# Kernel optimization log

Measured on AMD Instinct MI355X. Metric: run time of the kernel, lower is better.

## Reference

```python
import jax, jax.numpy as jnp
import numpy as np

D_IN = 4096
NUM_HEADS = 32
HEAD_DIM = 128
NUM_KV = 8
GROUP = NUM_HEADS // NUM_KV
EPS = 1e-6
ROPE_BASE = 10000.0


def rms_norm(x, scale):
    # norm over last dim (head_dim), computed in fp32 as in torch ref
    var = jnp.mean(x * x, axis=-1, keepdims=True)
    return x * jax.lax.rsqrt(var + EPS) * scale


def rope_cos_sin(positions, dim):
    inv_freq = 1.0 / (ROPE_BASE ** (jnp.arange(0, dim, 2, dtype=jnp.float32) / dim))
    angles = positions.astype(jnp.float32)[:, None] * inv_freq[None, :]  # (N, dim/2)
    angles = jnp.concatenate([angles, angles], axis=-1)  # (N, dim)
    return jnp.cos(angles), jnp.sin(angles)


def apply_rope(t, cos, sin):
    # t: (N, heads, D); cos/sin: (N, D)
    half = t.shape[-1] // 2
    rot = jnp.concatenate([-t[..., half:], t[..., :half]], axis=-1)
    return t * cos[:, None, :] + rot * sin[:, None, :]


def setup_inputs() -> dict:
    key = jax.random.key(0)
    ks = jax.random.split(key, 6)
    B, S = 1, 2048
    x = jax.random.normal(ks[0], (B, S, D_IN), dtype=jnp.float32)
    positions = jnp.arange(B * S, dtype=jnp.int32)
    sc = 0.02
    Wq = jax.random.normal(ks[1], (D_IN, NUM_HEADS * HEAD_DIM), dtype=jnp.float32) * sc
    Wk = jax.random.normal(ks[2], (D_IN, NUM_KV * HEAD_DIM), dtype=jnp.float32) * sc
    Wv = jax.random.normal(ks[3], (D_IN, NUM_KV * HEAD_DIM), dtype=jnp.float32) * sc
    Wo = jax.random.normal(ks[4], (NUM_HEADS * HEAD_DIM, D_IN), dtype=jnp.float32) * sc
    q_scale = jnp.ones((HEAD_DIM,), dtype=jnp.float32)
    k_scale = jnp.ones((HEAD_DIM,), dtype=jnp.float32)
    return {"x": x, "positions": positions, "Wq": Wq, "Wk": Wk, "Wv": Wv,
            "Wo": Wo, "q_scale": q_scale, "k_scale": k_scale}


def reference(x, positions, Wq, Wk, Wv, Wo, q_scale, k_scale):
    B, S, _ = x.shape
    N = B * S
    xf = x.reshape(N, D_IN)
    q = (xf @ Wq).reshape(N, NUM_HEADS, HEAD_DIM)
    k = (xf @ Wk).reshape(N, NUM_KV, HEAD_DIM)
    v = (xf @ Wv).reshape(N, NUM_KV, HEAD_DIM)
    # QK RMSNorm over head_dim
    q = rms_norm(q, q_scale)
    k = rms_norm(k, k_scale)
    # RoPE (rotate-half)
    cos, sin = rope_cos_sin(positions, HEAD_DIM)
    q = apply_rope(q, cos, sin)
    k = apply_rope(k, cos, sin)
    # (B, KV, group, S, D) for q; (B, KV, S, D) for k, v  (GQA broadcast)
    q = q.reshape(B, S, NUM_KV, GROUP, HEAD_DIM).transpose(0, 2, 3, 1, 4)
    k = k.reshape(B, S, NUM_KV, HEAD_DIM).transpose(0, 2, 1, 3)
    v = v.reshape(B, S, NUM_KV, HEAD_DIM).transpose(0, 2, 1, 3)
    scale = 1.0 / jnp.sqrt(jnp.float32(HEAD_DIM))
    scores = jnp.einsum('bghsd,bgtd->bghst', q, k) * scale  # (B,KV,G,S,S)
    causal = jnp.tril(jnp.ones((S, S), dtype=bool))
    scores = jnp.where(causal[None, None, None, :, :], scores, jnp.finfo(scores.dtype).min)
    attn = jax.nn.softmax(scores, axis=-1)
    ctx = jnp.einsum('bghst,bgtd->bghsd', attn, v)  # (B,KV,G,S,D)
    ctx = ctx.transpose(0, 3, 1, 2, 4).reshape(B, S, NUM_HEADS * HEAD_DIM)
    return ctx @ Wo
```

## Files before the change

kernel.cpp:

```cpp
#include <hip/hip_runtime.h>

#define S_LEN 2048
#define DMODEL 4096
#define NQKV 6144

typedef unsigned short u16;
typedef __attribute__((ext_vector_type(8))) short bf16x8;
typedef __attribute__((ext_vector_type(8))) unsigned short u16x8;
typedef __attribute__((ext_vector_type(4))) float f32x4;

#define NEG_BIG (-3.0e38f)

__device__ __forceinline__ float bf2f(u16 h) {
    union { unsigned u; float f; } c; c.u = ((unsigned)h) << 16; return c.f;
}
__device__ __forceinline__ u16 f2bf(float x) {
    union { float f; unsigned u; } c; c.f = x;
    return (u16)((c.u + 0x7fffu + ((c.u >> 16) & 1u)) >> 16);
}

__device__ __forceinline__ void gload16(const void* g, void* l) {
    __builtin_amdgcn_global_load_lds(
        (const __attribute__((address_space(1))) void*)g,
        (__attribute__((address_space(3))) void*)l, 16, 0, 0);
}

__device__ __forceinline__ void barfence() {
    asm volatile("" ::: "memory");
    __builtin_amdgcn_s_barrier();
    asm volatile("" ::: "memory");
}

__global__ __launch_bounds__(256) void detect_dtype(const u16* __restrict__ probe,
                                                    int* __restrict__ flags) {
    __shared__ int bad_s;
    if (threadIdx.x == 0) bad_s = 0;
    __syncthreads();
    int bad = 0;
    for (int i = threadIdx.x; i < 16384; i += 256) {
        float v = bf2f(probe[i]);
        if (!(fabsf(v) < 1e6f)) bad = 1;
    }
    if (bad) atomicOr(&bad_s, 1);
    __syncthreads();
    if (threadIdx.x == 0) { flags[0] = bad_s; flags[1] = 0; }
}

__global__ __launch_bounds__(256) void conv_bf16(const void* __restrict__ src,
                                                 u16* __restrict__ dst, long n,
                                                 const int* __restrict__ flag) {
    const bool f32 = (*flag != 0);
    long i = (long)blockIdx.x * 256 + threadIdx.x;
    long stride = (long)gridDim.x * 256;
    for (; i < n; i += stride) {
        float v = f32 ? ((const float*)src)[i] : bf2f(((const u16*)src)[i]);
        dst[i] = f2bf(v);
    }
}

__global__ __launch_bounds__(256) void transpose_any(
        const void* __restrict__ src, long base_off, long sld, long szoff,
        u16* __restrict__ dst, long dld, long dzoff,
        const int* __restrict__ flag) {
    __shared__ alignas(16) u16 tile[32][33];
    const bool f32 = (*flag != 0);
    u16* d = dst + (long)blockIdx.z * dzoff;
    long soff = base_off + (long)blockIdx.z * szoff;
    int c0 = blockIdx.x * 32, r0 = blockIdx.y * 32;
    int tx = threadIdx.x & 31, ty = threadIdx.x >> 5;
    for (int i = 0; i < 32; i += 8) {
        long idx = soff + (long)(r0 + ty + i) * sld + c0 + tx;
        float v = f32 ? ((const float*)src)[idx] : bf2f(((const u16*)src)[idx]);
        tile[ty + i][tx] = f2bf(v);
    }
    __syncthreads();
    for (int i = 0; i < 32; i += 8)
        d[(long)(c0 + ty + i) * dld + r0 + tx] = tile[tx][ty + i];
}

__device__ __forceinline__ void st_out(u16* C, size_t idx, float v)   { C[idx] = f2bf(v); }
__device__ __forceinline__ void st_out(float* C, size_t idx, float v) { C[idx] = v; }

template <typename OUT>
__device__ __forceinline__ void gemm_dp_core(
        const u16* __restrict__ A, const u16* __restrict__ BT,
        OUT* __restrict__ C, int K, int ldc) {
    __shared__ alignas(16) u16 smem[4 * 12288];
    const int tid = threadIdx.x;
    const int lane = tid & 63, wid = tid >> 6;
    const int wr = wid >> 1, wc = wid & 1;
    const int lm = lane & 15, lq = lane >> 4;
    const int m0 = blockIdx.y * 256, n0 = blockIdx.x * 128;

    const int cA0 = wid * 64 + lane;
    const int cA1 = 512 + cA0;
    const int cB  = wid * 64 + lane;
    const int rA0 = cA0 >> 2, rA1 = cA1 >> 2, rB = cB >> 2;
    const int spA0 = ((cA0 & 3) ^ ((rA0 >> 1) & 3)) * 8;
    const int spA1 = ((cA1 & 3) ^ ((rA1 >> 1) & 3)) * 8;
    const int spB  = ((cB  & 3) ^ ((rB  >> 1) & 3)) * 8;
    const u16* aS0 = A  + (size_t)(m0 + rA0) * K + spA0;
    const u16* aS1 = A  + (size_t)(m0 + rA1) * K + spA1;
    const u16* bS  = BT + (size_t)(n0 + rB ) * K + spB;
    const int ldsA0 = (wid * 64) * 8;
    const int ldsA1 = (512 + wid * 64) * 8;
    const int ldsB  = 8192 + (wid * 64) * 8;

    const int NK = K >> 5;
    for (int pt = 0; pt < 3; ++pt) {
        u16* buf = smem + pt * 12288;
        const int ko = pt << 5;
        gload16(aS0 + ko, buf + ldsA0);
        gload16(aS1 + ko, buf + ldsA1);
        gload16(bS  + ko, buf + ldsB);
    }
    asm volatile("s_waitcnt vmcnt(6)" ::: "memory");
    barfence();

    f32x4 acc[4][4] = {};
    const int arow = wr * 64 + lm;
    const int brow = wc * 64 + lm;

#pragma unroll 4
    for (int kt = 0; kt < NK; ++kt) {
        const u16* Ab = smem + (kt & 3) * 12288;
        const u16* Bb = Ab + 8192;
        bf16x8 bfv[4], afv[4];
        for (int ni = 0; ni < 4; ++ni) {
            int row = brow + ni * 16;
            bfv[ni] = *(const bf16x8*)(const void*)(Bb + row * 32 + ((lq ^ ((row >> 1) & 3)) << 3));
        }
        for (int mi = 0; mi < 4; ++mi) {
            int row = arow + mi * 16;
            afv[mi] = *(const bf16x8*)(const void*)(Ab + row * 32 + ((lq ^ ((row >> 1) & 3)) << 3));
        }
        if (kt + 3 < NK) {
            u16* nb = smem + ((kt + 3) & 3) * 12288;
            const int ko = (kt + 3) << 5;
            gload16(aS0 + ko, nb + ldsA0);
            gload16(aS1 + ko, nb + ldsA1);
            gload16(bS  + ko, nb + ldsB);
        }
        barfence();
        __builtin_amdgcn_s_setprio(1);
        for (int mi = 0; mi < 4; ++mi)
            for (int ni = 0; ni < 4; ++ni)
                acc[mi][ni] = __builtin_amdgcn_mfma_f32_16x16x32_bf16(afv[mi], bfv[ni], acc[mi][ni], 0, 0, 0);
        __builtin_amdgcn_s_setprio(0);
        if (kt + 3 < NK)       { asm volatile("s_waitcnt vmcnt(6)" ::: "memory"); }
        else if (kt + 2 < NK)  { asm volatile("s_waitcnt vmcnt(3)" ::: "memory"); }
        else if (kt + 1 < NK)  { asm volatile("s_waitcnt vmcnt(0)" ::: "memory"); }
        barfence();
    }

    for (int mi = 0; mi < 4; ++mi)
        for (int ni = 0; ni < 4; ++ni) {
            int col  = n0 + wc * 64 + ni * 16 + lm;
            int rowb = m0 + wr * 64 + mi * 16 + lq * 4;
            for (int r = 0; r < 4; ++r)
                st_out(C, (size_t)(rowb + r) * ldc + col, acc[mi][ni][r]);
        }
}

__global__ __launch_bounds__(512, 1) void gemm_dp_bf16(
        const u16* __restrict__ A, const u16* __restrict__ BT,
        u16* __restrict__ C, int K, int ldc) {
    gemm_dp_core<u16>(A, BT, C, K, ldc);
}
__global__ __launch_bounds__(512, 1) void gemm_dp_f32(
        const u16* __restrict__ A, const u16* __restrict__ BT,
        float* __restrict__ C, int K, int ldc) {
    gemm_dp_core<float>(A, BT, C, K, ldc);
}

__global__ __launch_bounds__(256) void rms_rope(
        const u16* __restrict__ qkv, const int* __restrict__ pos,
        const u16* __restrict__ qs, const u16* __restrict__ kscale,
        u16* __restrict__ Qb, u16* __restrict__ Kb) {
    int w = threadIdx.x >> 6, lane = threadIdx.x & 63;
    int task = blockIdx.x * 4 + w;
    int h = task >> 11, row = task & 2047;
    int base = (h < 32) ? h * 128 : 4096 + (h - 32) * 128;
    const u16* src = qkv + (size_t)row * NQKV + base;
    float t0 = bf2f(src[lane]), t1 = bf2f(src[lane + 64]);
    float ss = t0 * t0 + t1 * t1;
    for (int m = 1; m < 64; m <<= 1) ss += __shfl_xor(ss, m);
    float inv = rsqrtf(ss * (1.0f / 128.0f) + 1e-6f);
    const u16* sc = (h < 32) ? qs : kscale;
    float n0 = t0 * inv * bf2f(sc[lane]);
    float n1 = t1 * inv * bf2f(sc[lane + 64]);
    float p = (float)pos[row];
    float ang = p * __expf(-(float)lane * (9.210340371976184f / 64.0f));
    float c = cosf(ang), s = sinf(ang);
    float o0 = n0 * c - n1 * s;
    float o1 = n1 * c + n0 * s;
    float mul = (h < 32) ? 0.08838834764831845f : 1.0f;
    u16* dst = (h < 32) ? (Qb + ((size_t)h * S_LEN + row) * 128)
                        : (Kb + ((size_t)(h - 32) * S_LEN + row) * 128);
    dst[lane] = f2bf(o0 * mul);
    dst[lane + 64] = f2bf(o1 * mul);
}

__global__ __launch_bounds__(256, 2) void flash_attn(
        const u16* __restrict__ Qb, const u16* __restrict__ Kb,
        const u16* __restrict__ VTb, u16* __restrict__ ctx) {
    const int h = blockIdx.y, kvh = h >> 2;
    const int tid = threadIdx.x, lane = tid & 63, w = tid >> 6;
    const int lm = lane & 15, lq = lane >> 4;
    const int swz = (lm & 7) << 3;
    __shared__ alignas(16) u16 smem[20480];
    u16* Ksm = smem;
    u16* Vsm = smem + 8192;
    u16* Psm = smem + 16384;
    const u16* Kh = Kb + (size_t)kvh * S_LEN * 128;
    const u16* Vh = VTb + (size_t)kvh * 128 * S_LEN;

    for (int pass = 0; pass < 2; ++pass) {
        const int t = pass ? (31 - blockIdx.x) : blockIdx.x;
        const u16* Qh = Qb + ((size_t)h * S_LEN + (size_t)t * 64) * 128;

        __syncthreads();
        for (int i = 0; i < 4; ++i) {
            int g = i * 256 + tid;
            int row = g >> 4, s = g & 15;
            int sp = (s & 8) | ((s ^ row) & 7);
            gload16(Qh + (size_t)row * 128 + sp * 8,
                    Ksm + (size_t)(i * 256 + w * 64) * 8);
        }
        __syncthreads();
        bf16x8 aq[4];
        for (int ks = 0; ks < 4; ++ks)
            aq[ks] = *(const bf16x8*)(const void*)(
                Ksm + (((w * 16 + lm) * 128 + ks * 32 + lq * 8) ^ swz));

        float mrow[4], lrow[4];
        f32x4 accO[8];
        const f32x4 zero = {0.f, 0.f, 0.f, 0.f};
        for (int r = 0; r < 4; ++r) { mrow[r] = NEG_BIG; lrow[r] = 0.f; }
        for (int di = 0; di < 8; ++di) accO[di] = zero;

        for (int j = 0; j <= t; ++j) {
            __syncthreads();
            for (int i = 0; i < 4; ++i) {
                int g = i * 256 + tid;
                int row = g >> 4, s = g & 15;
                int sp = (s & 8) | ((s ^ row) & 7);
                gload16(Kh + (size_t)(j * 64 + row) * 128 + sp * 8,
                        Ksm + (size_t)(i * 256 + w * 64) * 8);
            }
            for (int i = 0; i < 4; ++i) {
                int g = i * 256 + tid;
                int d = g >> 3, s = g & 7;
                int sp = s ^ (d & 7);
                gload16(Vh + (size_t)d * S_LEN + j * 64 + sp * 8,
                        Vsm + (size_t)(i * 256 + w * 64) * 8);
            }
            __syncthreads();

            f32x4 sacc[4] = {};
            for (int ks = 0; ks < 4; ++ks) {
                bf16x8 kf[4];
                for (int ni = 0; ni < 4; ++ni)
                    kf[ni] = *(const bf16x8*)(const void*)(
                        Ksm + (((ni * 16 + lm) * 128 + ks * 32 + lq * 8) ^ swz));
                for (int ni = 0; ni < 4; ++ni)
                    sacc[ni] = __builtin_amdgcn_mfma_f32_16x16x32_bf16(aq[ks], kf[ni], sacc[ni], 0, 0, 0);
            }

            if (j == t) {
                for (int ni = 0; ni < 4; ++ni) {
                    int col = ni * 16 + lm;
                    for (int r = 0; r < 4; ++r)
                        if (col > w * 16 + lq * 4 + r) sacc[ni][r] = NEG_BIG;
                }
            }

            for (int r = 0; r < 4; ++r) {
                float mx = fmaxf(fmaxf(sacc[0][r], sacc[1][r]),
                                 fmaxf(sacc[2][r], sacc[3][r]));
                for (int sft = 1; sft < 16; sft <<= 1) mx = fmaxf(mx, __shfl_xor(mx, sft));
                float mN = fmaxf(mrow[r], mx);
                float alpha = __expf(mrow[r] - mN);
                mrow[r] = mN;
                float psum = 0.f;
                int prow = w * 16 + lq * 4 + r;
                for (int ni = 0; ni < 4; ++ni) {
                    float pv = __expf(sacc[ni][r] - mN);
                    psum += pv;
                    Psm[prow * 64 + ((ni * 16 + lm) ^ ((prow & 7) << 3))] = f2bf(pv);
                }
                for (int sft = 1; sft < 16; sft <<= 1) psum += __shfl_xor(psum, sft);
                lrow[r] = lrow[r] * alpha + psum;
                for (int di = 0; di < 8; ++di) accO[di][r] *= alpha;
            }
            __syncthreads();

            for (int ks2 = 0; ks2 < 2; ++ks2) {
                bf16x8 pf = *(const bf16x8*)(const void*)(
                    Psm + (((w * 16 + lm) * 64 + ks2 * 32 + lq * 8) ^ swz));
                for (int di = 0; di < 8; ++di) {
                    bf16x8 vf = *(const bf16x8*)(const void*)(
                        Vsm + (((di * 16 + lm) * 64 + ks2 * 32 + lq * 8) ^ swz));
                    accO[di] = __builtin_amdgcn_mfma_f32_16x16x32_bf16(pf, vf, accO[di], 0, 0, 0);
                }
            }
        }

        for (int r = 0; r < 4; ++r) {
            float invl = 1.0f / fmaxf(lrow[r], 1e-30f);
            size_t rowg = (size_t)t * 64 + w * 16 + lq * 4 + r;
            for (int di = 0; di < 8; ++di)
                ctx[rowg * 4096 + h * 128 + di * 16 + lm] = f2bf(accO[di][r] * invl);
        }
    }
}

extern "C" void kernel_launch(void* const* d_in, const int* in_sizes, int n_in,
                              void* d_out, int out_size, void* d_ws, size_t ws_size,
                              hipStream_t stream) {
    const void* x   = d_in[0];
    const int* pos  = (const int*)d_in[1];
    const void* Wq  = d_in[2];
    const void* Wk  = d_in[3];
    const void* Wv  = d_in[4];
    const void* Wo  = d_in[5];
    const void* qs  = d_in[6];
    const void* ks  = d_in[7];

    if (ws_size < (size_t)145 * 1024 * 1024) return;
    char* ws = (char*)d_ws;
    u16* WqkvT = (u16*)ws;
    u16* WoT   = (u16*)(ws + (size_t)48  * 1024 * 1024);
    u16* qkv   = (u16*)(ws + (size_t)80  * 1024 * 1024);
    u16* ctx   = qkv;
    u16* Qb    = (u16*)(ws + (size_t)104 * 1024 * 1024);
    u16* Kb    = (u16*)(ws + (size_t)120 * 1024 * 1024);
    u16* VTb   = (u16*)(ws + (size_t)124 * 1024 * 1024);
    u16* xb    = (u16*)(ws + (size_t)128 * 1024 * 1024);
    int* flags = (int*)(ws + (size_t)144 * 1024 * 1024);
    u16* qsb   = (u16*)(ws + (size_t)144 * 1024 * 1024 + 1024);
    u16* ksb   = (u16*)(ws + (size_t)144 * 1024 * 1024 + 2048);

    dim3 b256(256);
    const int* flag  = flags;
    const int* fzero = flags + 1;

    detect_dtype<<<1, b256, 0, stream>>>((const u16*)Wq, flags);
    conv_bf16<<<8192, b256, 0, stream>>>(x,  xb,  (long)S_LEN * DMODEL, flag);
    conv_bf16<<<1,    b256, 0, stream>>>(qs, qsb, 128, flag);
    conv_bf16<<<1,    b256, 0, stream>>>(ks, ksb, 128, flag);

    transpose_any<<<dim3(128, 128, 1), b256, 0, stream>>>(Wq, 0, 4096, 0, WqkvT, 4096, 0, flag);
    transpose_any<<<dim3(32, 128, 1),  b256, 0, stream>>>(Wk, 0, 1024, 0, WqkvT + (size_t)4096 * 4096, 4096, 0, flag);
    transpose_any<<<dim3(32, 128, 1),  b256, 0, stream>>>(Wv, 0, 1024, 0, WqkvT + (size_t)5120 * 4096, 4096, 0, flag);
    transpose_any<<<dim3(128, 128, 1), b256, 0, stream>>>(Wo, 0, 4096, 0, WoT, 4096, 0, flag);

    gemm_dp_bf16<<<dim3(48, 8), dim3(512), 0, stream>>>(xb, WqkvT, qkv, 4096, NQKV);
    rms_rope<<<dim3(20480), b256, 0, stream>>>(qkv, pos, qsb, ksb, Qb, Kb);
    transpose_any<<<dim3(4, 64, 8), b256, 0, stream>>>(qkv, 5120, NQKV, 128, VTb, 2048, (long)128 * 2048, fzero);
    flash_attn<<<dim3(16, 32), b256, 0, stream>>>(Qb, Kb, VTb, ctx);
    gemm_dp_f32<<<dim3(32, 8), dim3(512), 0, stream>>>(ctx, WoT, (float*)d_out, 4096, 4096);
}
```

Before: 573.0 us.

## Rewrite GEMM core with 256x256 tiles, BK=64 double buffering and interleaved loads

Replaces the 256x128, BK=32, 4-stage GEMM with a 256x256 block tile and a K-step of 64 using two LDS buffers. Each wave now computes a 128x64 sub-tile. Next-tile global-to-LDS loads are interleaved between MFMA groups within an iteration. This raises arithmetic intensity and cuts LDS traffic per flop, but halves the grid (192 and 128 blocks on a 256-CU part), which risks leaving CUs idle. Launch bounds change to 2 blocks per CU even though 128KB of LDS per block likely prevents co-residency.

```diff
diff --git a/kernel.cpp b/kernel.cpp
--- a/kernel.cpp
+++ b/kernel.cpp
@@ -30,6 +30,8 @@
     __builtin_amdgcn_s_barrier();
     asm volatile("" ::: "memory");
 }
+
+#define MFMA16(d, av, bv) d = __builtin_amdgcn_mfma_f32_16x16x32_bf16(av, bv, d, 0, 0, 0)
 
 __global__ __launch_bounds__(256) void detect_dtype(const u16* __restrict__ probe,
                                                     int* __restrict__ flags) {
@@ -82,95 +84,139 @@
 __device__ __forceinline__ void st_out(float* C, size_t idx, float v) { C[idx] = v; }
 
 template <typename OUT>
-__device__ __forceinline__ void gemm_dp_core(
+__device__ __forceinline__ void gemm_dp2_core(
         const u16* __restrict__ A, const u16* __restrict__ BT,
         OUT* __restrict__ C, int K, int ldc) {
-    __shared__ alignas(16) u16 smem[4 * 12288];
+    __shared__ alignas(16) u16 smem[65536];
     const int tid = threadIdx.x;
     const int lane = tid & 63, wid = tid >> 6;
-    const int wr = wid >> 1, wc = wid & 1;
+    const int wr = wid >> 2, wc = wid & 3;
     const int lm = lane & 15, lq = lane >> 4;
-    const int m0 = blockIdx.y * 256, n0 = blockIdx.x * 128;
-
-    const int cA0 = wid * 64 + lane;
-    const int cA1 = 512 + cA0;
-    const int cB  = wid * 64 + lane;
-    const int rA0 = cA0 >> 2, rA1 = cA1 >> 2, rB = cB >> 2;
-    const int spA0 = ((cA0 & 3) ^ ((rA0 >> 1) & 3)) * 8;
-    const int spA1 = ((cA1 & 3) ^ ((rA1 >> 1) & 3)) * 8;
-    const int spB  = ((cB  & 3) ^ ((rB  >> 1) & 3)) * 8;
-    const u16* aS0 = A  + (size_t)(m0 + rA0) * K + spA0;
-    const u16* aS1 = A  + (size_t)(m0 + rA1) * K + spA1;
-    const u16* bS  = BT + (size_t)(n0 + rB ) * K + spB;
-    const int ldsA0 = (wid * 64) * 8;
-    const int ldsA1 = (512 + wid * 64) * 8;
-    const int ldsB  = 8192 + (wid * 64) * 8;
-
-    const int NK = K >> 5;
-    for (int pt = 0; pt < 3; ++pt) {
-        u16* buf = smem + pt * 12288;
-        const int ko = pt << 5;
-        gload16(aS0 + ko, buf + ldsA0);
-        gload16(aS1 + ko, buf + ldsA1);
-        gload16(bS  + ko, buf + ldsB);
+    const int m0 = blockIdx.y * 256, n0 = blockIdx.x * 256;
+
+    const int srow = tid >> 3;
+    const int sgrp = (tid & 7) ^ (srow & 7);
+    const u16* aS = A  + (size_t)(m0 + srow) * K + sgrp * 8;
+    const u16* bS = BT + (size_t)(n0 + srow) * K + sgrp * 8;
+    u16* ldsA = smem + tid * 8;
+    u16* ldsB = smem + 16384 + tid * 8;
+
+    auto stA = [&](int bufi, int c, int kti) {
+        gload16(aS + (size_t)c * 64 * K + (size_t)kti * 64, ldsA + bufi * 32768 + c * 4096);
+    };
+    auto stB = [&](int bufi, int c, int kti) {
+        gload16(bS + (size_t)c * 64 * K + (size_t)kti * 64, ldsB + bufi * 32768 + c * 4096);
+    };
+    auto rdA = [&](const u16* buf, int mi, int ks) {
+        int row = wr * 128 + mi * 16 + lm;
+        return *(const bf16x8*)(const void*)(buf + row * 64 + (((ks * 4 + lq) ^ (row & 7)) << 3));
+    };
+    auto rdB = [&](const u16* buf, int ni, int ks) {
+        int row = wc * 64 + ni * 16 + lm;
+        return *(const bf16x8*)(const void*)(buf + 16384 + row * 64 + (((ks * 4 + lq) ^ (row & 7)) << 3));
+    };
+
+    const int NK = K >> 6;
+    stB(0, 0, 0); stB(0, 1, 0); stB(0, 2, 0); stB(0, 3, 0);
+    stA(0, 0, 0); stA(0, 2, 0); stA(0, 1, 0); stA(0, 3, 0);
+
+    f32x4 acc[8][4] = {};
+    bf16x8 b[4][2], a[2][2];
+
+#pragma unroll 2
+    for (int kt = 0; kt < NK; ++kt) {
+        const u16* buf = smem + (kt & 1) * 32768;
+        const int nb = (kt & 1) ^ 1;
+        const int kn = kt + 1;
+        const bool more = kn < NK;
+
+        asm volatile("s_waitcnt vmcnt(2)" ::: "memory");
+        barfence();
+#pragma unroll
+        for (int ni = 0; ni < 4; ++ni)
+#pragma unroll
+            for (int ks = 0; ks < 2; ++ks) b[ni][ks] = rdB(buf, ni, ks);
+#pragma unroll
+        for (int q = 0; q < 2; ++q)
+#pragma unroll
+            for (int ks = 0; ks < 2; ++ks) a[q][ks] = rdA(buf, q, ks);
+        if (more) { stB(nb, 0, kn); stB(nb, 1, kn); }
+        __builtin_amdgcn_s_setprio(1);
+#pragma unroll
+        for (int q = 0; q < 2; ++q)
+#pragma unroll
+            for (int ni = 0; ni < 4; ++ni)
+#pragma unroll
+                for (int ks = 0; ks < 2; ++ks) MFMA16(acc[q][ni], a[q][ks], b[ni][ks]);
+        __builtin_amdgcn_s_setprio(0);
+
+#pragma unroll
+        for (int q = 0; q < 2; ++q)
+#pragma unroll
+            for (int ks = 0; ks < 2; ++ks) a[q][ks] = rdA(buf, 2 + q, ks);
+        if (more) { stB(nb, 2, kn); stB(nb, 3, kn); }
+        __builtin_amdgcn_s_setprio(1);
+#pragma unroll
+        for (int q = 0; q < 2; ++q)
+#pragma unroll
+            for (int ni = 0; ni < 4; ++ni)
+#pragma unroll
+                for (int ks = 0; ks < 2; ++ks) MFMA16(acc[2 + q][ni], a[q][ks], b[ni][ks]);
+        __builtin_amdgcn_s_setprio(0);
+
+        if (more) { asm volatile("s_waitcnt vmcnt(4)" ::: "memory"); }
+        else      { asm volatile("s_waitcnt vmcnt(0)" ::: "memory"); }
+        barfence();
+#pragma unroll
+        for (int q = 0; q < 2; ++q)
+#pragma unroll
+            for (int ks = 0; ks < 2; ++ks) a[q][ks] = rdA(buf, 4 + q, ks);
+        if (more) { stA(nb, 0, kn); stA(nb, 2, kn); }
+        __builtin_amdgcn_s_setprio(1);
+#pragma unroll
+        for (int q = 0; q < 2; ++q)
+#pragma unroll
+            for (int ni = 0; ni < 4; ++ni)
+#pragma unroll
+                for (int ks = 0; ks < 2; ++ks) MFMA16(acc[4 + q][ni], a[q][ks], b[ni][ks]);
+        __builtin_amdgcn_s_setprio(0);
+
+#pragma unroll
+        for (int q = 0; q < 2; ++q)
+#pragma unroll
+            for (int ks = 0; ks < 2; ++ks) a[q][ks] = rdA(buf, 6 + q, ks);
+        if (more) { stA(nb, 1, kn); stA(nb, 3, kn); }
+        __builtin_amdgcn_s_setprio(1);
+#pragma unroll
+        for (int q = 0; q < 2; ++q)
+#pragma unroll
+            for (int ni = 0; ni < 4; ++ni)
+#pragma unroll
+                for (int ks = 0; ks < 2; ++ks) MFMA16(acc[6 + q][ni], a[q][ks], b[ni][ks]);
+        __builtin_amdgcn_s_setprio(0);
     }
-    asm volatile("s_waitcnt vmcnt(6)" ::: "memory");
-    barfence();
-
-    f32x4 acc[4][4] = {};
-    const int arow = wr * 64 + lm;
-    const int brow = wc * 64 + lm;
-
-#pragma unroll 4
-    for (int kt = 0; kt < NK; ++kt) {
-        const u16* Ab = smem + (kt & 3) * 12288;
-        const u16* Bb = Ab + 8192;
-        bf16x8 bfv[4], afv[4];
-        for (int ni = 0; ni < 4; ++ni) {
-            int row = brow + ni * 16;
-            bfv[ni] = *(const bf16x8*)(const void*)(Bb + row * 32 + ((lq ^ ((row >> 1) & 3)) << 3));
-        }
-        for (int mi = 0; mi < 4; ++mi) {
-            int row = arow + mi * 16;
-            afv[mi] = *(const bf16x8*)(const void*)(Ab + row * 32 + ((lq ^ ((row >> 1) & 3)) << 3));
-        }
-        if (kt + 3 < NK) {
-            u16* nb = smem + ((kt + 3) & 3) * 12288;
-            const int ko = (kt + 3) << 5;
-            gload16(aS0 + ko, nb + ldsA0);
-            gload16(aS1 + ko, nb + ldsA1);
-            gload16(bS  + ko, nb + ldsB);
-        }
-        barfence();
-        __builtin_amdgcn_s_setprio(1);
-        for (int mi = 0; mi < 4; ++mi)
-            for (int ni = 0; ni < 4; ++ni)
-                acc[mi][ni] = __builtin_amdgcn_mfma_f32_16x16x32_bf16(afv[mi], bfv[ni], acc[mi][ni], 0, 0, 0);
-        __builtin_amdgcn_s_setprio(0);
-        if (kt + 3 < NK)       { asm volatile("s_waitcnt vmcnt(6)" ::: "memory"); }
-        else if (kt + 2 < NK)  { asm volatile("s_waitcnt vmcnt(3)" ::: "memory"); }
-        else if (kt + 1 < NK)  { asm volatile("s_waitcnt vmcnt(0)" ::: "memory"); }
-        barfence();
-    }
-
-    for (int mi = 0; mi < 4; ++mi)
+
+#pragma unroll
+    for (int mi = 0; mi < 8; ++mi)
+#pragma unroll
         for (int ni = 0; ni < 4; ++ni) {
             int col  = n0 + wc * 64 + ni * 16 + lm;
-            int rowb = m0 + wr * 64 + mi * 16 + lq * 4;
+            int rowb = m0 + wr * 128 + mi * 16 + lq * 4;
+#pragma unroll
             for (int r = 0; r < 4; ++r)
                 st_out(C, (size_t)(rowb + r) * ldc + col, acc[mi][ni][r]);
         }
 }
 
-__global__ __launch_bounds__(512, 1) void gemm_dp_bf16(
+__global__ __launch_bounds__(512, 2) void gemm_dp2_bf16(
         const u16* __restrict__ A, const u16* __restrict__ BT,
         u16* __restrict__ C, int K, int ldc) {
-    gemm_dp_core<u16>(A, BT, C, K, ldc);
-}
-__global__ __launch_bounds__(512, 1) void gemm_dp_f32(
+    gemm_dp2_core<u16>(A, BT, C, K, ldc);
+}
+__global__ __launch_bounds__(512, 2) void gemm_dp2_f32(
         const u16* __restrict__ A, const u16* __restrict__ BT,
         float* __restrict__ C, int K, int ldc) {
-    gemm_dp_core<float>(A, BT, C, K, ldc);
+    gemm_dp2_core<float>(A, BT, C, K, ldc);
 }
 
 __global__ __launch_bounds__(256) void rms_rope(
@@ -355,9 +401,9 @@
     transpose_any<<<dim3(32, 128, 1),  b256, 0, stream>>>(Wv, 0, 1024, 0, WqkvT + (size_t)5120 * 4096, 4096, 0, flag);
     transpose_any<<<dim3(128, 128, 1), b256, 0, stream>>>(Wo, 0, 4096, 0, WoT, 4096, 0, flag);
 
-    gemm_dp_bf16<<<dim3(48, 8), dim3(512), 0, stream>>>(xb, WqkvT, qkv, 4096, NQKV);
+    gemm_dp2_bf16<<<dim3(24, 8), dim3(512), 0, stream>>>(xb, WqkvT, qkv, 4096, NQKV);
     rms_rope<<<dim3(20480), b256, 0, stream>>>(qkv, pos, qsb, ksb, Qb, Kb);
     transpose_any<<<dim3(4, 64, 8), b256, 0, stream>>>(qkv, 5120, NQKV, 128, VTb, 2048, (long)128 * 2048, fzero);
     flash_attn<<<dim3(16, 32), b256, 0, stream>>>(Qb, Kb, VTb, ctx);
-    gemm_dp_f32<<<dim3(32, 8), dim3(512), 0, stream>>>(ctx, WoT, (float*)d_out, 4096, 4096);
-}
+    gemm_dp2_f32<<<dim3(16, 8), dim3(512), 0, stream>>>(ctx, WoT, (float*)d_out, 4096, 4096);
+}
```

Result: faster. 561.4 us (-2.0%).
